# Kernel optimization log

Measured on AMD Instinct MI355X. Metric: run time of the kernel, lower is better.

## Reference

```python
import jax, jax.numpy as jnp
import numpy as np

L = 1.0          # diffusion coefficient `l`
CHUNK = 1024     # tile size over the blurred-pixel axis


def _conv(x, k):
    # x: [B,H,W,C], k: [kh,kw,C,F] -> [B,H,W,F]; equivalent to the source's
    # NCHW/OIHW transposed conv with 'SAME' padding, stride 1.
    return jax.lax.conv_general_dilated(
        x, k, window_strides=(1, 1), padding='SAME',
        dimension_numbers=('NHWC', 'HWIO', 'NHWC'))


def _difference(x, blurred):
    # difference[b,i,j,k] = sum_{p,q,f} tanh(x[b,i,j,k] - blurred[b,p,q,f])
    # Computed in CHUNK-sized tiles over the blurred axis to avoid the
    # [B, H*W*C, H*W*F] all-pairs tensor the nested vmaps would materialize.
    b = x.shape[0]
    xf = x.reshape(b, -1)                              # [B, M]
    yf = blurred.reshape(b, -1)                        # [B, N]
    n = yf.shape[1]
    pad = (-n) % CHUNK
    yf = jnp.pad(yf, ((0, 0), (0, pad)))
    mask = jnp.pad(jnp.ones((n,), x.dtype), (0, pad))
    ychunks = yf.reshape(b, -1, CHUNK).transpose(1, 0, 2)   # [S, B, CHUNK]
    mchunks = mask.reshape(-1, CHUNK)                        # [S, CHUNK]

    def step(acc, ym):
        yc, mc = ym
        d = jnp.tanh(xf[:, :, None] - yc[:, None, :])        # [B, M, CHUNK]
        return acc + jnp.einsum('bmn,n->bm', d, mc), None

    acc, _ = jax.lax.scan(step, jnp.zeros_like(xf), (ychunks, mchunks))
    return acc.reshape(x.shape)                              # [B,H,W,C]


def setup_inputs() -> dict:
    key = jax.random.key(0)
    k1, k2, k3, k4 = jax.random.split(key, 4)
    lecun = 1.0 / np.sqrt(5 * 5 * 3)  # fan_in of the 5x5x3 kernels
    return {
        'inputs': jax.random.normal(k1, (2, 32, 32, 3), dtype=jnp.float32),
        'm': jax.random.normal(k2, (5, 5, 3, 16), dtype=jnp.float32) * lecun,
        'w': jax.random.normal(k3, (5, 5, 3, 16), dtype=jnp.float32) * lecun,
        'g': jax.random.normal(k4, (5, 5, 3, 16), dtype=jnp.float32) * lecun,
    }


def reference(inputs, m, w, g):
    first_term = _conv(inputs, m)          # [B,H,W,F]
    blurred = _conv(inputs, g)             # [B,H,W,F]
    difference = _difference(inputs, blurred)  # [B,H,W,C]
    second_term = _conv(difference, w)     # [B,H,W,F]
    return first_term - L * second_term
```

## Files before the change

### kernel.cpp

```cpp
#include <hip/hip_runtime.h>

#define BB 2
#define HH 32
#define WW 32
#define CC 3
#define FF 16
#define M_PER_B (HH*WW*CC)
#define N_PER_B (HH*WW*FF)
#define CHN 256
#define NCHUNKS (N_PER_B / CHN)
#define MBLOCKS (M_PER_B / 256)

__global__ __launch_bounds__(256) void diff_kernel(
    const float* __restrict__ x,
    const float* __restrict__ gk,
    float* __restrict__ dacc)
{
    __shared__ float ys2[CHN];
    const int tid = threadIdx.x;
    const int b   = blockIdx.z;
    const int mb  = blockIdx.x;
    const int nc  = blockIdx.y;

    {
        int n = nc * CHN + tid;
        int p = n >> 9;
        int r = n & 511;
        int q = r >> 4;
        int f = r & 15;
        float acc = 0.f;
        #pragma unroll
        for (int dh = 0; dh < 5; ++dh) {
            int hh = p + dh - 2;
            if ((unsigned)hh >= (unsigned)HH) continue;
            #pragma unroll
            for (int dw = 0; dw < 5; ++dw) {
                int ww = q + dw - 2;
                if ((unsigned)ww >= (unsigned)WW) continue;
                const float* xin = x  + ((b*HH + hh)*WW + ww)*CC;
                const float* gg  = gk + ((dh*5 + dw)*CC)*FF + f;
                #pragma unroll
                for (int c = 0; c < CC; ++c)
                    acc += xin[c] * gg[c*FF];
            }
        }
        ys2[tid] = 2.0f * acc;
    }
    __syncthreads();

    const int m = mb * 256 + tid;
    const float x2 = 2.0f * x[b*M_PER_B + m];
    float s = 0.f;
    #pragma unroll 8
    for (int n = 0; n < CHN; ++n) {
        float e = __expf(x2 - ys2[n]);
        s += __builtin_amdgcn_rcpf(1.0f + e);
    }
    atomicAdd(&dacc[b*M_PER_B + m], -2.0f * s);
}

__global__ __launch_bounds__(256) void out_kernel(
    const float* __restrict__ x,
    const float* __restrict__ mker,
    const float* __restrict__ wker,
    const float* __restrict__ dacc,
    float* __restrict__ out)
{
    int o = blockIdx.x * 256 + threadIdx.x;
    int f = o & 15;
    int t = o >> 4;
    int j = t & 31;  t >>= 5;
    int i = t & 31;  t >>= 5;
    int b = t;
    float ft = 0.f, st = 0.f;
    #pragma unroll
    for (int dh = 0; dh < 5; ++dh) {
        int hh = i + dh - 2;
        if ((unsigned)hh >= (unsigned)HH) continue;
        #pragma unroll
        for (int dw = 0; dw < 5; ++dw) {
            int ww = j + dw - 2;
            if ((unsigned)ww >= (unsigned)WW) continue;
            int base = ((b*HH + hh)*WW + ww)*CC;
            int kb   = ((dh*5 + dw)*CC)*FF + f;
            #pragma unroll
            for (int c = 0; c < CC; ++c) {
                ft += x[base + c] * mker[kb + c*FF];
                st += (16384.0f + dacc[base + c]) * wker[kb + c*FF];
            }
        }
    }
    out[o] = ft - st;
}

extern "C" void kernel_launch(void* const* d_in, const int* in_sizes, int n_in,
                              void* d_out, int out_size, void* d_ws, size_t ws_size,
                              hipStream_t stream) {
    const float* x  = (const float*)d_in[0];
    const float* mk = (const float*)d_in[1];
    const float* wk = (const float*)d_in[2];
    const float* gk = (const float*)d_in[3];
    float* out  = (float*)d_out;
    float* dacc = (float*)d_ws;

    hipMemsetAsync(dacc, 0, BB*M_PER_B*sizeof(float), stream);
    diff_kernel<<<dim3(MBLOCKS, NCHUNKS, BB), 256, 0, stream>>>(x, gk, dacc);
    out_kernel<<<(BB*HH*WW*FF)/256, 256, 0, stream>>>(x, mk, wk, dacc, out);
}
```

Measured before the change: 99.31 us.

## Factor the tanh exponential and pair reciprocals in the all-pairs kernel

Rewrites exp(2x-2y) as exp(2x)*exp(-2y), so each exponential is computed once per x element and once per blurred element instead of once per pair. Two terms are then combined over a shared denominator, 1/a+1/b = (a+b)/(ab), which halves the reciprocal count. Each thread also handles two m elements so every shared-memory load is reused twice, which halves the number of blocks. This cuts transcendental throughput pressure in the dominant all-pairs loop. In exchange, the products can overflow for large x-y gaps and produce inf*0 = NaN, which is safe only while input magnitudes stay moderate.

```diff
diff --git a/kernel.cpp b/kernel.cpp
--- a/kernel.cpp
+++ b/kernel.cpp
@@ -9,18 +9,24 @@
 #define N_PER_B (HH*WW*FF)
 #define CHN 256
 #define NCHUNKS (N_PER_B / CHN)
-#define MBLOCKS (M_PER_B / 256)
+#define MPT 2
+#define MBLOCKS (M_PER_B / (256*MPT))
 
 __global__ __launch_bounds__(256) void diff_kernel(
     const float* __restrict__ x,
     const float* __restrict__ gk,
     float* __restrict__ dacc)
 {
-    __shared__ float ys2[CHN];
+    __shared__ float Fs[CHN];
     const int tid = threadIdx.x;
     const int b   = blockIdx.z;
     const int mb  = blockIdx.x;
     const int nc  = blockIdx.y;
+
+    const int m0 = mb * (256*MPT) + tid;
+    const int m1 = m0 + 256;
+    const float E0 = __expf(2.0f * x[b*M_PER_B + m0]);
+    const float E1 = __expf(2.0f * x[b*M_PER_B + m1]);
 
     {
         int n = nc * CHN + tid;
@@ -44,19 +50,24 @@
                     acc += xin[c] * gg[c*FF];
             }
         }
-        ys2[tid] = 2.0f * acc;
+        Fs[tid] = __expf(-2.0f * acc);
     }
     __syncthreads();
 
-    const int m = mb * 256 + tid;
-    const float x2 = 2.0f * x[b*M_PER_B + m];
-    float s = 0.f;
-    #pragma unroll 8
-    for (int n = 0; n < CHN; ++n) {
-        float e = __expf(x2 - ys2[n]);
-        s += __builtin_amdgcn_rcpf(1.0f + e);
+    float s0 = 0.f, s1 = 0.f;
+    #pragma unroll 4
+    for (int n = 0; n < CHN; n += 2) {
+        float f0 = Fs[n];
+        float f1 = Fs[n+1];
+        float a0 = fmaf(E0, f0, 1.0f);
+        float b0 = fmaf(E0, f1, 1.0f);
+        float a1 = fmaf(E1, f0, 1.0f);
+        float b1 = fmaf(E1, f1, 1.0f);
+        s0 += (a0 + b0) * __builtin_amdgcn_rcpf(a0 * b0);
+        s1 += (a1 + b1) * __builtin_amdgcn_rcpf(a1 * b1);
     }
-    atomicAdd(&dacc[b*M_PER_B + m], -2.0f * s);
+    atomicAdd(&dacc[b*M_PER_B + m0], -2.0f * s0);
+    atomicAdd(&dacc[b*M_PER_B + m1], -2.0f * s1);
 }
 
 __global__ __launch_bounds__(256) void out_kernel(
```

New measurement: 83.86 us. -15.6%, faster.
